# Performance work log

Measured on AMD Instinct MI355X. Metric: run time of the kernel, lower is better.

The kernel has to match this reference:

```python
import jax, jax.numpy as jnp
import numpy as np

HEADS = 16
KV_HEADS = 8
HEAD_DIM = 128
ROPE_BASE = 10000.0
RMS_EPS = 1e-5


def rmsnorm(x, w, eps=RMS_EPS):
    x = jnp.clip(x.astype(jnp.float32), -100.0, 100.0)
    var = jnp.clip(jnp.mean(x * x, axis=-1, keepdims=True), eps, None)
    x = x * jax.lax.rsqrt(var + eps)
    x = jnp.clip(x, -10.0, 10.0)
    return w * x


def activation_quant(x):
    x = jnp.clip(x, -50.0, 50.0)
    max_val = jnp.clip(jnp.max(jnp.abs(x), axis=-1, keepdims=True), 0.0001, None)
    scale = 127.0 / max_val
    return jnp.clip(jnp.round(x * scale), -128.0, 127.0) / scale


def weight_quant(w):
    scale = jnp.clip(jnp.mean(jnp.abs(w)), 1e-8, None)
    e = jnp.mean(w)
    return jnp.sign(w - e) * scale


def bitlinear(x, w, norm_w):
    xn = rmsnorm(x, norm_w)
    xq = xn + jax.lax.stop_gradient(activation_quant(xn) - xn)
    wq = w + jax.lax.stop_gradient(weight_quant(w) - w)
    return xq @ wq.T


def rope_tables(seq_len, dim):
    inv_freq = 1.0 / (ROPE_BASE ** (jnp.arange(0, dim, 2, dtype=jnp.float32) / dim))
    freqs = jnp.outer(jnp.arange(seq_len, dtype=jnp.float32), inv_freq)  # [S, dim/2]
    emb = jnp.concatenate([freqs, freqs], axis=-1)  # [S, dim]
    return jnp.cos(emb), jnp.sin(emb)


def rotate_half(x):
    x1, x2 = jnp.split(x, 2, axis=-1)
    return jnp.concatenate([-x2, x1], axis=-1)


def attention_forward(hidden_states, attention_mask, wq, wk, wv, wo, nq, nk, nv, no):
    B, S, H = hidden_states.shape
    q = bitlinear(hidden_states, wq, nq)  # [B,S,nh*hd]
    k = bitlinear(hidden_states, wk, nk)  # [B,S,nkv*hd]
    v = bitlinear(hidden_states, wv, nv)

    q = q.reshape(B, S, HEADS, HEAD_DIM).transpose(0, 2, 1, 3)       # [B,nh,S,hd]
    k = k.reshape(B, S, KV_HEADS, HEAD_DIM).transpose(0, 2, 1, 3)    # [B,nkv,S,hd]
    v = v.reshape(B, S, KV_HEADS, HEAD_DIM).transpose(0, 2, 1, 3)

    cos, sin = rope_tables(S, HEAD_DIM)
    cos = cos[None, None]  # [1,1,S,hd]
    sin = sin[None, None]
    q = q * cos + rotate_half(q) * sin
    k = k * cos + rotate_half(k) * sin

    groups = HEADS // KV_HEADS
    k_exp = jnp.repeat(k, groups, axis=1)  # [B,nh,S,hd]
    v_exp = jnp.repeat(v, groups, axis=1)

    scale = 1.0 / jnp.sqrt(jnp.float32(HEAD_DIM))
    scores = jnp.einsum('bhqd,bhkd->bhqk', q, k_exp) * scale
    scores = scores + attention_mask
    attn = jax.nn.softmax(scores, axis=-1)
    out = jnp.einsum('bhqk,bhkd->bhqd', attn, v_exp)
    out = out.transpose(0, 2, 1, 3).reshape(B, S, HEADS * HEAD_DIM)
    return bitlinear(out, wo, no)


def setup_inputs() -> dict:
    key = jax.random.key(0)
    ks = jax.random.split(key, 6)
    B, S, H = 2, 2048, 2048
    KVH = KV_HEADS * HEAD_DIM
    std = 0.02 / np.sqrt(H)
    return {
        'hidden_states': jax.random.normal(ks[0], (B, S, H), jnp.float32),
        'attention_mask': jnp.zeros((1, 1, S, S), jnp.float32),
        'wq': jax.random.normal(ks[1], (H, H), jnp.float32) * std,
        'wk': jax.random.normal(ks[2], (KVH, H), jnp.float32) * std,
        'wv': jax.random.normal(ks[3], (KVH, H), jnp.float32) * std,
        'wo': jax.random.normal(ks[4], (H, H), jnp.float32) * std,
        'nq': jnp.ones((H,), jnp.float32),
        'nk': jnp.ones((H,), jnp.float32),
        'nv': jnp.ones((H,), jnp.float32),
        'no': jnp.ones((H,), jnp.float32),
    }


def reference(hidden_states, attention_mask, wq, wk, wv, wo, nq, nk, nv, no):
    return attention_forward(hidden_states, attention_mask, wq, wk, wv, wo, nq, nk, nv, no)
```

## Files before the change

### kernel.cpp

```cpp
#include <hip/hip_runtime.h>


#define DI __device__ __forceinline__

using bf16   = __bf16;
using bf16x4 = __attribute__((ext_vector_type(4))) __bf16;
using bf16x8 = __attribute__((ext_vector_type(8))) __bf16;
using f32x4  = __attribute__((ext_vector_type(4))) float;

DI void gl_lds16(void* lds, const void* g) {
  __builtin_amdgcn_global_load_lds((const __attribute__((address_space(1))) void*)g,
                                   (__attribute__((address_space(3))) void*)lds, 16, 0, 0);
}
DI float clampf(float x, float lo, float hi) { return fminf(fmaxf(x, lo), hi); }

DI float block_sum(float v, float* red, int lane, int w) {
#pragma unroll
  for (int o = 32; o > 0; o >>= 1) v += __shfl_xor(v, o, 64);
  __syncthreads();
  if (lane == 0) red[w] = v;
  __syncthreads();
  return red[0] + red[1] + red[2] + red[3];
}
DI float block_max(float v, float* red, int lane, int w) {
#pragma unroll
  for (int o = 32; o > 0; o >>= 1) v = fmaxf(v, __shfl_xor(v, o, 64));
  __syncthreads();
  if (lane == 0) red[w] = v;
  __syncthreads();
  return fmaxf(fmaxf(red[0], red[1]), fmaxf(red[2], red[3]));
}

__global__ void wstats_kernel(const float* wq, const float* wk, const float* wv,
                              const float* wo, float* stats) {
  __shared__ float red[4], red2[4];
  int t = threadIdx.x, lane = t & 63, w = t >> 6;
  int m = blockIdx.y;
  const float* src; int n4;
  if (m == 0)      { src = wq; n4 = 1048576; }
  else if (m == 1) { src = wk; n4 = 524288;  }
  else if (m == 2) { src = wv; n4 = 524288;  }
  else             { src = wo; n4 = 1048576; }
  float s = 0.f, sa = 0.f;
  for (int i = blockIdx.x * 256 + t; i < n4; i += 256 * 256) {
    float4 v = ((const float4*)src)[i];
    s  += v.x + v.y + v.z + v.w;
    sa += fabsf(v.x) + fabsf(v.y) + fabsf(v.z) + fabsf(v.w);
  }
#pragma unroll
  for (int o = 32; o > 0; o >>= 1) { s += __shfl_xor(s, o, 64); sa += __shfl_xor(sa, o, 64); }
  if (lane == 0) { red[w] = s; red2[w] = sa; }
  __syncthreads();
  if (t == 0) {
    atomicAdd(&stats[2 * m],     red[0] + red[1] + red[2] + red[3]);
    atomicAdd(&stats[2 * m + 1], red2[0] + red2[1] + red2[2] + red2[3]);
  }
}

__global__ void wsign_kernel(const float* wq, const float* wk, const float* wv, const float* wo,
                             ushort* sq, ushort* sk, ushort* sv, ushort* so,
                             const float* stats) {
  int m = blockIdx.y;
  const float* src; ushort* dst; int n4; float cinv;
  if (m == 0)      { src = wq; dst = sq; n4 = 1048576; cinv = 1.f / 4194304.f; }
  else if (m == 1) { src = wk; dst = sk; n4 = 524288;  cinv = 1.f / 2097152.f; }
  else if (m == 2) { src = wv; dst = sv; n4 = 524288;  cinv = 1.f / 2097152.f; }
  else             { src = wo; dst = so; n4 = 1048576; cinv = 1.f / 4194304.f; }
  float e = stats[2 * m] * cinv;
  for (int i = blockIdx.x * 256 + threadIdx.x; i < n4; i += 1024 * 256) {
    float4 v = ((const float4*)src)[i];
    ushort4 o;
    o.x = v.x > e ? 0x3F80 : (v.x < e ? 0xBF80 : 0);
    o.y = v.y > e ? 0x3F80 : (v.y < e ? 0xBF80 : 0);
    o.z = v.z > e ? 0x3F80 : (v.z < e ? 0xBF80 : 0);
    o.w = v.w > e ? 0x3F80 : (v.w < e ? 0xBF80 : 0);
    ((ushort4*)dst)[i] = o;
  }
}

__global__ void ropetab_kernel(float* ct, float* st) {
  int s = blockIdx.x, j = threadIdx.x;
  float invf = powf(10000.f, -(float)j * (1.f / 64.f));
  float a = (float)s * invf;
  ct[s * 64 + j] = cosf(a);
  st[s * 64 + j] = sinf(a);
}

DI void quant_one(const float* xs, const float* __restrict__ wt, bf16* __restrict__ a,
                  float* __restrict__ r, int row, int t, int lane, int w, float* red) {
  float4 w0 = ((const float4*)wt)[t * 2], w1 = ((const float4*)wt)[t * 2 + 1];
  float wv[8] = {w0.x, w0.y, w0.z, w0.w, w1.x, w1.y, w1.z, w1.w};
  float y[8]; float am = 0.f;
#pragma unroll
  for (int e = 0; e < 8; ++e) {
    y[e] = clampf(wv[e] * xs[e], -50.f, 50.f);
    am = fmaxf(am, fabsf(y[e]));
  }
  float mx = block_max(am, red, lane, w);
  float maxval = fmaxf(mx, 1e-4f);
  float sc = 127.f / maxval;
  bf16x8 q;
#pragma unroll
  for (int e = 0; e < 8; ++e) {
    float n = rintf(y[e] * sc);
    n = clampf(n, -128.f, 127.f);
    q[e] = (bf16)n;
  }
  *(bf16x8*)(a + (size_t)row * 2048 + t * 8) = q;
  if (t == 0) r[row] = maxval * (1.f / 127.f);
}

template <int NW>
__launch_bounds__(256)
__global__ void rqnorm_kernel(const float* __restrict__ x,
                              const float* __restrict__ w0, const float* __restrict__ w1,
                              const float* __restrict__ w2,
                              bf16* a0, bf16* a1, bf16* a2,
                              float* r0, float* r1, float* r2) {
  __shared__ float red[4];
  int t = threadIdx.x, lane = t & 63, w = t >> 6;
  int row = blockIdx.x;
  const float* xr = x + (size_t)row * 2048;
  float4 u0 = ((const float4*)xr)[t * 2], u1 = ((const float4*)xr)[t * 2 + 1];
  float xs[8] = {u0.x, u0.y, u0.z, u0.w, u1.x, u1.y, u1.z, u1.w};
  float ss = 0.f;
#pragma unroll
  for (int e = 0; e < 8; ++e) { xs[e] = clampf(xs[e], -100.f, 100.f); ss += xs[e] * xs[e]; }
  float tot = block_sum(ss, red, lane, w);
  float var = fmaxf(tot * (1.f / 2048.f), 1e-5f);
  float inv = 1.f / sqrtf(var + 1e-5f);
#pragma unroll
  for (int e = 0; e < 8; ++e) xs[e] = clampf(xs[e] * inv, -10.f, 10.f);
  quant_one(xs, w0, a0, r0, row, t, lane, w, red);
  if (NW > 1) quant_one(xs, w1, a1, r1, row, t, lane, w, red);
  if (NW > 2) quant_one(xs, w2, a2, r2, row, t, lane, w, red);
}

DI void mm_core(const bf16* __restrict__ Ag0, const bf16* __restrict__ Bg0,
                bf16* As, bf16* Bs, int w, int lane, f32x4 acc[2][8]) {
  int l15 = lane & 15, quad = lane >> 4;
  int srow = w * 8 + (lane >> 3);
  int sc_p = (lane & 7) * 8;
  int sc_g = ((lane & 7) ^ (lane >> 3)) * 8;
  const bf16* Ag = Ag0 + (size_t)srow * 2048 + sc_g;
  const bf16* Bg = Bg0 + (size_t)srow * 2048 + sc_g;
  bf16* Al = As + srow * 64 + sc_p;
  bf16* Bl = Bs + srow * 64 + sc_p;
  for (int kt = 0; kt < 32; ++kt) {
    size_t kb = (size_t)kt * 64;
#pragma unroll
    for (int i = 0; i < 4; ++i) {
      gl_lds16(Al + i * 32 * 64, Ag + (size_t)i * 32 * 2048 + kb);
      gl_lds16(Bl + i * 32 * 64, Bg + (size_t)i * 32 * 2048 + kb);
    }
    __syncthreads();
#pragma unroll
    for (int kc = 0; kc < 2; ++kc) {
      bf16x8 af[2], bfr[8];
#pragma unroll
      for (int mt = 0; mt < 2; ++mt)
        af[mt] = *(const bf16x8*)(As + (w * 32 + mt * 16 + l15) * 64 +
                                  (((kc * 4 + quad) ^ (l15 & 7)) * 8));
#pragma unroll
      for (int nt = 0; nt < 8; ++nt)
        bfr[nt] = *(const bf16x8*)(Bs + (nt * 16 + l15) * 64 +
                                   (((kc * 4 + quad) ^ (l15 & 7)) * 8));
#pragma unroll
      for (int mt = 0; mt < 2; ++mt)
#pragma unroll
        for (int nt = 0; nt < 8; ++nt)
          acc[mt][nt] = __builtin_amdgcn_mfma_f32_16x16x32_bf16(af[mt], bfr[nt], acc[mt][nt], 0, 0, 0);
    }
    __syncthreads();
  }
}

__launch_bounds__(256, 2)
__global__ void qkv_gemm(const bf16* __restrict__ Aq, const bf16* __restrict__ Ak,
                         const bf16* __restrict__ Av, const bf16* __restrict__ Ball,
                         const float* __restrict__ rq, const float* __restrict__ rk,
                         const float* __restrict__ rv, const float* __restrict__ stats,
                         bf16* __restrict__ qr, bf16* __restrict__ kr,
                         float* __restrict__ vlin,
                         const float* __restrict__ ct, const float* __restrict__ st) {
  __shared__ bf16 As[128 * 64];
  __shared__ bf16 Bs[128 * 64];
  int t = threadIdx.x, w = t >> 6, lane = t & 63;
  int l15 = lane & 15, quad = lane >> 4;
  int x = blockIdx.x, m0 = blockIdx.y * 128;
  const bf16* A; const float* rs; float sw; int brow0;
  if (x < 16)      { A = Aq; rs = rq; sw = stats[1] * (1.f / 4194304.f); brow0 = x * 128; }
  else if (x < 24) { A = Ak; rs = rk; sw = stats[3] * (1.f / 2097152.f); brow0 = 2048 + (x - 16) * 128; }
  else             { A = Av; rs = rv; sw = stats[5] * (1.f / 2097152.f); brow0 = 3072 + (x - 24) * 128; }
  sw = fmaxf(sw, 1e-8f);
  f32x4 acc[2][8] = {};
  mm_core(A + (size_t)m0 * 2048, Ball + (size_t)brow0 * 2048, As, Bs, w, lane, acc);

  if (x < 24) {
    bf16* outb = (x < 16) ? qr : kr;
    int h = (x < 16) ? x : x - 16;
    int nh = (x < 16) ? 16 : 8;
#pragma unroll
    for (int mt = 0; mt < 2; ++mt)
#pragma unroll
      for (int r = 0; r < 4; ++r) {
        int row = m0 + w * 32 + mt * 16 + quad * 4 + r;
        float rsc = rs[row] * sw;
        int s = row & 2047, b = row >> 11;
        size_t base = ((size_t)(b * nh + h) * 2048 + s) * 128;
#pragma unroll
        for (int nt = 0; nt < 4; ++nt) {
          int d = nt * 16 + l15;
          float x1 = acc[mt][nt][r] * rsc;
          float x2 = acc[mt][nt + 4][r] * rsc;
          float c = ct[s * 64 + d], sn = st[s * 64 + d];
          outb[base + d]      = (bf16)(x1 * c - x2 * sn);
          outb[base + d + 64] = (bf16)(x2 * c + x1 * sn);
        }
      }
  } else {
    int n0 = (x - 24) * 128;
#pragma unroll
    for (int mt = 0; mt < 2; ++mt)
#pragma unroll
      for (int r = 0; r < 4; ++r) {
        int row = m0 + w * 32 + mt * 16 + quad * 4 + r;
        float rsc = rs[row] * sw;
#pragma unroll
        for (int nt = 0; nt < 8; ++nt)
          vlin[(size_t)row * 1024 + n0 + nt * 16 + l15] = acc[mt][nt][r] * rsc;
      }
  }
}

__launch_bounds__(256, 2)
__global__ void gemm_o(const bf16* __restrict__ A, const bf16* __restrict__ Bw,
                       const float* __restrict__ rs, const float* __restrict__ stats,
                       float* __restrict__ out) {
  __shared__ bf16 As[128 * 64];
  __shared__ bf16 Bs[128 * 64];
  int t = threadIdx.x, w = t >> 6, lane = t & 63;
  int l15 = lane & 15, quad = lane >> 4;
  int m0 = blockIdx.y * 128, n0 = blockIdx.x * 128;
  f32x4 acc[2][8] = {};
  mm_core(A + (size_t)m0 * 2048, Bw + (size_t)n0 * 2048, As, Bs, w, lane, acc);
  float sw = fmaxf(stats[7] * (1.f / 4194304.f), 1e-8f);
#pragma unroll
  for (int mt = 0; mt < 2; ++mt)
#pragma unroll
    for (int r = 0; r < 4; ++r) {
      int row = m0 + w * 32 + mt * 16 + quad * 4 + r;
      float rsc = rs[row] * sw;
#pragma unroll
      for (int nt = 0; nt < 8; ++nt)
        out[(size_t)row * 2048 + n0 + nt * 16 + l15] = acc[mt][nt][r] * rsc;
    }
}

__global__ void vtrans_kernel(const float* __restrict__ v_lin, bf16* __restrict__ v_t) {
  __shared__ float tile[64][65];
  int t = threadIdx.x, c = t & 63, rq = t >> 6;
  int ct0 = blockIdx.x * 64, tt0 = blockIdx.y * 64;
#pragma unroll
  for (int i = 0; i < 16; ++i) {
    int r = rq * 16 + i;
    tile[r][c] = v_lin[(size_t)(tt0 + r) * 1024 + ct0 + c];
  }
  __syncthreads();
  int token = tt0 + c;
  int b = token >> 11, s = token & 2047;
#pragma unroll
  for (int i = 0; i < 16; ++i) {
    int cg = ct0 + rq * 16 + i;
    int kvh = cg >> 7, d = cg & 127;
    v_t[((size_t)(b * 8 + kvh) * 128 + d) * 2048 + s] = (bf16)tile[c][rq * 16 + i];
  }
}

__launch_bounds__(256, 2)
__global__ void attn_kernel(const bf16* __restrict__ Q, const bf16* __restrict__ Kc,
                            const bf16* __restrict__ Vt, const float* __restrict__ mask,
                            float* __restrict__ Oout) {
  constexpr float scale = 0.08838834764831845f;
  __shared__ bf16 Ks[2][64 * 128];
  __shared__ bf16 Vs[2][128 * 64];
  __shared__ bf16 Ps[128 * 64];
  int t = threadIdx.x, w = t >> 6, lane = t & 63;
  int l15 = lane & 15, quad = lane >> 4;
  int bh = blockIdx.y, b = bh >> 4, h = bh & 15, kvh = h >> 1;
  int q0 = blockIdx.x * 128;
  const bf16* Qb = Q + (size_t)(b * 16 + h) * 2048 * 128;
  const bf16* Kb = Kc + (size_t)(b * 8 + kvh) * 2048 * 128;
  const bf16* Vb = Vt + (size_t)(b * 8 + kvh) * 128 * 2048;

  int qloc = w * 32 + l15;
  int qg = q0 + qloc;

  bf16x8 qf[2][4];
#pragma unroll
  for (int qt = 0; qt < 2; ++qt)
#pragma unroll
    for (int kc = 0; kc < 4; ++kc)
      qf[qt][kc] = *(const bf16x8*)(Qb + (size_t)(qg + qt * 16) * 128 + kc * 32 + quad * 8);

  f32x4 Oa[8][2] = {};
  float mrow[2] = {-1e30f, -1e30f}, lrow[2] = {0.f, 0.f};

  int krow = w * 4 + quad;
  int kcol_p = l15 * 8;
  int kcol_g = (l15 ^ krow) * 8;
  int vrow = w * 8 + (lane >> 3);
  int vc_p = (lane & 7) * 8;
  int vc_g = ((lane & 7) ^ (lane >> 3)) * 8;

  auto stage = [&](int buf, int kt) {
    int kk0 = kt * 64;
#pragma unroll
    for (int i = 0; i < 4; ++i)
      gl_lds16(&Ks[buf][(i * 16 + krow) * 128 + kcol_p],
               Kb + (size_t)(kk0 + i * 16 + krow) * 128 + kcol_g);
#pragma unroll
    for (int i = 0; i < 4; ++i)
      gl_lds16(&Vs[buf][(i * 32 + vrow) * 64 + vc_p],
               Vb + (size_t)(i * 32 + vrow) * 2048 + kk0 + vc_g);
  };

  stage(0, 0);

  f32x4 mv[2][4], mvn[2][4];
#pragma unroll
  for (int qt = 0; qt < 2; ++qt)
#pragma unroll
    for (int k2 = 0; k2 < 4; ++k2)
      mv[qt][k2] = *(const f32x4*)(mask + (size_t)(qg + qt * 16) * 2048 + k2 * 16 + quad * 4);

  for (int kt = 0; kt < 32; ++kt) {
    int cur = kt & 1;
    __syncthreads();
    if (kt < 31) stage(cur ^ 1, kt + 1);

    f32x4 Sacc[4][2] = {};
#pragma unroll
    for (int kc = 0; kc < 4; ++kc) {
      bf16x8 kf[4];
#pragma unroll
      for (int k2 = 0; k2 < 4; ++k2)
        kf[k2] = *(const bf16x8*)(&Ks[cur][(k2 * 16 + l15) * 128 + (((kc * 4 + quad) ^ l15) * 8)]);
#pragma unroll
      for (int k2 = 0; k2 < 4; ++k2)
#pragma unroll
        for (int qt = 0; qt < 2; ++qt)
          Sacc[k2][qt] = __builtin_amdgcn_mfma_f32_16x16x32_bf16(kf[k2], qf[qt][kc], Sacc[k2][qt], 0, 0, 0);
    }

#pragma unroll
    for (int qt = 0; qt < 2; ++qt) {
#pragma unroll
      for (int k2 = 0; k2 < 4; ++k2)
#pragma unroll
        for (int r = 0; r < 4; ++r)
          Sacc[k2][qt][r] = Sacc[k2][qt][r] * scale + mv[qt][k2][r];
      f32x4 vm = Sacc[0][qt];
#pragma unroll
      for (int k2 = 1; k2 < 4; ++k2)
#pragma unroll
        for (int r = 0; r < 4; ++r) vm[r] = fmaxf(vm[r], Sacc[k2][qt][r]);
      float mx = fmaxf(fmaxf(vm[0], vm[1]), fmaxf(vm[2], vm[3]));
      mx = fmaxf(mx, __shfl_xor(mx, 16, 64));
      mx = fmaxf(mx, __shfl_xor(mx, 32, 64));
      float mnew = fmaxf(mrow[qt], mx);
      float alpha = __expf(mrow[qt] - mnew);
      mrow[qt] = mnew;
      f32x4 vs = {0.f, 0.f, 0.f, 0.f};
#pragma unroll
      for (int k2 = 0; k2 < 4; ++k2)
#pragma unroll
        for (int r = 0; r < 4; ++r) {
          float p = __expf(Sacc[k2][qt][r] - mnew);
          Sacc[k2][qt][r] = p;
          vs[r] += p;
        }
      float rsum = (vs[0] + vs[1]) + (vs[2] + vs[3]);
      rsum += __shfl_xor(rsum, 16, 64);
      rsum += __shfl_xor(rsum, 32, 64);
      lrow[qt] = lrow[qt] * alpha + rsum;
#pragma unroll
      for (int dt = 0; dt < 8; ++dt) Oa[dt][qt] *= alpha;
      int qr = qloc + qt * 16;
#pragma unroll
      for (int k2 = 0; k2 < 4; ++k2) {
        bf16x4 pk;
#pragma unroll
        for (int r = 0; r < 4; ++r) pk[r] = (bf16)Sacc[k2][qt][r];
        int c = k2 * 2 + (quad >> 1);
        *(bf16x4*)(&Ps[qr * 64 + ((c ^ (qr & 7)) * 8) + (quad & 1) * 4]) = pk;
      }
    }

    if (kt < 31) {
      int kk1 = (kt + 1) * 64;
#pragma unroll
      for (int qt = 0; qt < 2; ++qt)
#pragma unroll
        for (int k2 = 0; k2 < 4; ++k2)
          mvn[qt][k2] = *(const f32x4*)(mask + (size_t)(qg + qt * 16) * 2048 + kk1 + k2 * 16 + quad * 4);
    }

#pragma unroll
    for (int kc = 0; kc < 2; ++kc) {
      bf16x8 pf[2];
#pragma unroll
      for (int qt = 0; qt < 2; ++qt)
        pf[qt] = *(const bf16x8*)(&Ps[(qloc + qt * 16) * 64 + (((kc * 4 + quad) ^ (l15 & 7)) * 8)]);
#pragma unroll
      for (int dt = 0; dt < 8; ++dt) {
        bf16x8 vf = *(const bf16x8*)(&Vs[cur][(dt * 16 + l15) * 64 +
                                              (((kc * 4 + quad) ^ (l15 & 7)) * 8)]);
#pragma unroll
        for (int qt = 0; qt < 2; ++qt)
          Oa[dt][qt] = __builtin_amdgcn_mfma_f32_16x16x32_bf16(vf, pf[qt], Oa[dt][qt], 0, 0, 0);
      }
    }

#pragma unroll
    for (int qt = 0; qt < 2; ++qt)
#pragma unroll
      for (int k2 = 0; k2 < 4; ++k2) mv[qt][k2] = mvn[qt][k2];
  }

#pragma unroll
  for (int qt = 0; qt < 2; ++qt) {
    float inv = 1.f / lrow[qt];
    int token = b * 2048 + qg + qt * 16;
#pragma unroll
    for (int dt = 0; dt < 8; ++dt) {
      f32x4 o = Oa[dt][qt] * inv;
      *(f32x4*)(Oout + (size_t)token * 2048 + h * 128 + dt * 16 + quad * 4) = o;
    }
  }
}

extern "C" void kernel_launch(void* const* d_in, const int* in_sizes, int n_in,
                              void* d_out, int out_size, void* d_ws, size_t ws_size,
                              hipStream_t stream) {
  const float* hidden = (const float*)d_in[0];
  const float* mask   = (const float*)d_in[1];
  const float* wq = (const float*)d_in[2];
  const float* wk = (const float*)d_in[3];
  const float* wv = (const float*)d_in[4];
  const float* wo = (const float*)d_in[5];
  const float* nq = (const float*)d_in[6];
  const float* nk = (const float*)d_in[7];
  const float* nv = (const float*)d_in[8];
  const float* no = (const float*)d_in[9];
  float* out = (float*)d_out;
  char* ws = (char*)d_ws;

  constexpr size_t O_STATS = 0;
  constexpr size_t O_CT    = 256;
  constexpr size_t O_ST    = O_CT + 524288;
  constexpr size_t O_SQ    = O_ST + 524288;
  constexpr size_t O_SK    = O_SQ + 8388608;
  constexpr size_t O_SV    = O_SK + 4194304;
  constexpr size_t O_SO    = O_SV + 4194304;
  constexpr size_t O_RSQ   = O_SO + 8388608;
  constexpr size_t O_RSK   = O_RSQ + 16384;
  constexpr size_t O_RSV   = O_RSK + 16384;
  constexpr size_t O_RSO   = O_RSV + 16384;
  constexpr size_t O_AQQ   = O_RSO + 16384;
  constexpr size_t O_AQK   = O_AQQ + 16777216;
  constexpr size_t O_AQV   = O_AQK + 16777216;
  constexpr size_t O_QR    = O_AQV + 16777216;
  constexpr size_t O_KR    = O_QR + 16777216;
  constexpr size_t O_VT    = O_KR + 8388608;
  constexpr size_t O_VLIN2 = O_VT + 8388608;
  constexpr size_t O_ATTN  = O_AQQ;
  constexpr size_t O_AQO   = O_AQV;

  float* stats = (float*)(ws + O_STATS);
  float* ct = (float*)(ws + O_CT);
  float* st = (float*)(ws + O_ST);

  (void)hipMemsetAsync(ws + O_STATS, 0, 256, stream);

  wstats_kernel<<<dim3(256, 4), 256, 0, stream>>>(wq, wk, wv, wo, stats);
  wsign_kernel<<<dim3(1024, 4), 256, 0, stream>>>(wq, wk, wv, wo,
      (ushort*)(ws + O_SQ), (ushort*)(ws + O_SK), (ushort*)(ws + O_SV), (ushort*)(ws + O_SO), stats);
  ropetab_kernel<<<dim3(2048), 64, 0, stream>>>(ct, st);

  rqnorm_kernel<3><<<dim3(4096), 256, 0, stream>>>(hidden, nq, nk, nv,
      (bf16*)(ws + O_AQQ), (bf16*)(ws + O_AQK), (bf16*)(ws + O_AQV),
      (float*)(ws + O_RSQ), (float*)(ws + O_RSK), (float*)(ws + O_RSV));

  qkv_gemm<<<dim3(32, 32), 256, 0, stream>>>(
      (const bf16*)(ws + O_AQQ), (const bf16*)(ws + O_AQK), (const bf16*)(ws + O_AQV),
      (const bf16*)(ws + O_SQ),
      (const float*)(ws + O_RSQ), (const float*)(ws + O_RSK), (const float*)(ws + O_RSV),
      stats, (bf16*)(ws + O_QR), (bf16*)(ws + O_KR), (float*)(ws + O_VLIN2), ct, st);

  vtrans_kernel<<<dim3(16, 64), 256, 0, stream>>>((const float*)(ws + O_VLIN2), (bf16*)(ws + O_VT));

  attn_kernel<<<dim3(16, 32), 256, 0, stream>>>(
      (const bf16*)(ws + O_QR), (const bf16*)(ws + O_KR), (const bf16*)(ws + O_VT),
      mask, (float*)(ws + O_ATTN));

  rqnorm_kernel<1><<<dim3(4096), 256, 0, stream>>>((const float*)(ws + O_ATTN), no, no, no,
      (bf16*)(ws + O_AQO), (bf16*)(ws + O_AQO), (bf16*)(ws + O_AQO),
      (float*)(ws + O_RSO), (float*)(ws + O_RSO), (float*)(ws + O_RSO));

  gemm_o<<<dim3(16, 32), 256, 0, stream>>>(
      (const bf16*)(ws + O_AQO), (const bf16*)(ws + O_SO), (float*)(ws + O_RSO), stats, out);

  (void)in_sizes; (void)n_in; (void)out_size; (void)ws_size;
}
```

Measured before the change: 437.3 us.

## Fuse V transpose into QKV GEMM epilogue and shrink attention tiles

The V projection epilogue now writes bf16 directly in the transposed [b,kvh,d,s] layout, which removes the fp32 intermediate buffer and the separate transpose kernel. The attention kernel moves from 128 to 64 query rows per block and from 64 to 32 keys per iteration. That gives one query tile per wave, less LDS per block, launch bounds raised to 4 blocks per SM, and twice as many blocks. The cost is more loop iterations, more K/V reloads per query (each block covers fewer queries), and smaller MFMA batches per sync.

```diff
diff --git a/kernel.cpp b/kernel.cpp
--- a/kernel.cpp
+++ b/kernel.cpp
@@ -181,7 +181,7 @@
                          const float* __restrict__ rq, const float* __restrict__ rk,
                          const float* __restrict__ rv, const float* __restrict__ stats,
                          bf16* __restrict__ qr, bf16* __restrict__ kr,
-                         float* __restrict__ vlin,
+                         bf16* __restrict__ vt_out,
                          const float* __restrict__ ct, const float* __restrict__ st) {
   __shared__ bf16 As[128 * 64];
   __shared__ bf16 Bs[128 * 64];
@@ -219,17 +219,24 @@
         }
       }
   } else {
-    int n0 = (x - 24) * 128;
-#pragma unroll
-    for (int mt = 0; mt < 2; ++mt)
-#pragma unroll
-      for (int r = 0; r < 4; ++r) {
-        int row = m0 + w * 32 + mt * 16 + quad * 4 + r;
-        float rsc = rs[row] * sw;
-#pragma unroll
-        for (int nt = 0; nt < 8; ++nt)
-          vlin[(size_t)row * 1024 + n0 + nt * 16 + l15] = acc[mt][nt][r] * rsc;
+    int n0x = (x - 24) * 128;
+#pragma unroll
+    for (int mt = 0; mt < 2; ++mt) {
+      int token0 = m0 + w * 32 + mt * 16 + quad * 4;
+      float rsc[4];
+#pragma unroll
+      for (int r = 0; r < 4; ++r) rsc[r] = rs[token0 + r] * sw;
+      int bb = token0 >> 11, s0 = token0 & 2047;
+#pragma unroll
+      for (int nt = 0; nt < 8; ++nt) {
+        int col = n0x + nt * 16 + l15;
+        int kvh2 = col >> 7, d = col & 127;
+        bf16x4 pv;
+#pragma unroll
+        for (int r = 0; r < 4; ++r) pv[r] = (bf16)(acc[mt][nt][r] * rsc[r]);
+        *(bf16x4*)(vt_out + ((size_t)(bb * 8 + kvh2) * 128 + d) * 2048 + s0) = pv;
       }
+    }
   }
 }
 
@@ -257,186 +264,137 @@
     }
 }
 
-__global__ void vtrans_kernel(const float* __restrict__ v_lin, bf16* __restrict__ v_t) {
-  __shared__ float tile[64][65];
-  int t = threadIdx.x, c = t & 63, rq = t >> 6;
-  int ct0 = blockIdx.x * 64, tt0 = blockIdx.y * 64;
-#pragma unroll
-  for (int i = 0; i < 16; ++i) {
-    int r = rq * 16 + i;
-    tile[r][c] = v_lin[(size_t)(tt0 + r) * 1024 + ct0 + c];
-  }
-  __syncthreads();
-  int token = tt0 + c;
-  int b = token >> 11, s = token & 2047;
-#pragma unroll
-  for (int i = 0; i < 16; ++i) {
-    int cg = ct0 + rq * 16 + i;
-    int kvh = cg >> 7, d = cg & 127;
-    v_t[((size_t)(b * 8 + kvh) * 128 + d) * 2048 + s] = (bf16)tile[c][rq * 16 + i];
-  }
-}
-
-__launch_bounds__(256, 2)
+__launch_bounds__(256, 4)
 __global__ void attn_kernel(const bf16* __restrict__ Q, const bf16* __restrict__ Kc,
                             const bf16* __restrict__ Vt, const float* __restrict__ mask,
                             float* __restrict__ Oout) {
   constexpr float scale = 0.08838834764831845f;
-  __shared__ bf16 Ks[2][64 * 128];
-  __shared__ bf16 Vs[2][128 * 64];
-  __shared__ bf16 Ps[128 * 64];
+  __shared__ bf16 Ks[2][32 * 128];
+  __shared__ bf16 Vs[2][128 * 32];
+  __shared__ bf16 Ps[64 * 40];
   int t = threadIdx.x, w = t >> 6, lane = t & 63;
   int l15 = lane & 15, quad = lane >> 4;
   int bh = blockIdx.y, b = bh >> 4, h = bh & 15, kvh = h >> 1;
-  int q0 = blockIdx.x * 128;
+  int q0 = blockIdx.x * 64;
   const bf16* Qb = Q + (size_t)(b * 16 + h) * 2048 * 128;
   const bf16* Kb = Kc + (size_t)(b * 8 + kvh) * 2048 * 128;
   const bf16* Vb = Vt + (size_t)(b * 8 + kvh) * 128 * 2048;
 
-  int qloc = w * 32 + l15;
+  int qloc = w * 16 + l15;
   int qg = q0 + qloc;
 
-  bf16x8 qf[2][4];
-#pragma unroll
-  for (int qt = 0; qt < 2; ++qt)
-#pragma unroll
-    for (int kc = 0; kc < 4; ++kc)
-      qf[qt][kc] = *(const bf16x8*)(Qb + (size_t)(qg + qt * 16) * 128 + kc * 32 + quad * 8);
-
-  f32x4 Oa[8][2] = {};
-  float mrow[2] = {-1e30f, -1e30f}, lrow[2] = {0.f, 0.f};
-
-  int krow = w * 4 + quad;
-  int kcol_p = l15 * 8;
-  int kcol_g = (l15 ^ krow) * 8;
-  int vrow = w * 8 + (lane >> 3);
-  int vc_p = (lane & 7) * 8;
-  int vc_g = ((lane & 7) ^ (lane >> 3)) * 8;
+  bf16x8 qf[4];
+#pragma unroll
+  for (int kc = 0; kc < 4; ++kc)
+    qf[kc] = *(const bf16x8*)(Qb + (size_t)qg * 128 + kc * 32 + quad * 8);
+
+  f32x4 Oa[8] = {};
+  float mrow = -1e30f, lrow = 0.f;
+
+  int ksr = t >> 4;
+  int ksc_p = (t & 15) * 8;
+  int ksc_g = ((t & 15) ^ ksr) * 8;
+  int vsr = t >> 2;
+  int vsc_p = (t & 3) * 8;
+  int vsc_g = ((t & 3) ^ (vsr & 3)) * 8;
 
   auto stage = [&](int buf, int kt) {
-    int kk0 = kt * 64;
-#pragma unroll
-    for (int i = 0; i < 4; ++i)
-      gl_lds16(&Ks[buf][(i * 16 + krow) * 128 + kcol_p],
-               Kb + (size_t)(kk0 + i * 16 + krow) * 128 + kcol_g);
-#pragma unroll
-    for (int i = 0; i < 4; ++i)
-      gl_lds16(&Vs[buf][(i * 32 + vrow) * 64 + vc_p],
-               Vb + (size_t)(i * 32 + vrow) * 2048 + kk0 + vc_g);
+    int kk0 = kt * 32;
+#pragma unroll
+    for (int i = 0; i < 2; ++i)
+      gl_lds16(&Ks[buf][(i * 16 + ksr) * 128 + ksc_p],
+               Kb + (size_t)(kk0 + i * 16 + ksr) * 128 + ksc_g);
+#pragma unroll
+    for (int i = 0; i < 2; ++i)
+      gl_lds16(&Vs[buf][(i * 64 + vsr) * 32 + vsc_p],
+               Vb + (size_t)(i * 64 + vsr) * 2048 + kk0 + vsc_g);
   };
 
   stage(0, 0);
 
-  f32x4 mv[2][4], mvn[2][4];
-#pragma unroll
-  for (int qt = 0; qt < 2; ++qt)
-#pragma unroll
-    for (int k2 = 0; k2 < 4; ++k2)
-      mv[qt][k2] = *(const f32x4*)(mask + (size_t)(qg + qt * 16) * 2048 + k2 * 16 + quad * 4);
-
-  for (int kt = 0; kt < 32; ++kt) {
+  f32x4 mv[2], mvn[2];
+#pragma unroll
+  for (int k2 = 0; k2 < 2; ++k2)
+    mv[k2] = *(const f32x4*)(mask + (size_t)qg * 2048 + k2 * 16 + quad * 4);
+
+  for (int kt = 0; kt < 64; ++kt) {
     int cur = kt & 1;
     __syncthreads();
-    if (kt < 31) stage(cur ^ 1, kt + 1);
-
-    f32x4 Sacc[4][2] = {};
+    if (kt < 63) stage(cur ^ 1, kt + 1);
+
+    f32x4 Sacc[2] = {};
 #pragma unroll
     for (int kc = 0; kc < 4; ++kc) {
-      bf16x8 kf[4];
-#pragma unroll
-      for (int k2 = 0; k2 < 4; ++k2)
+      bf16x8 kf[2];
+#pragma unroll
+      for (int k2 = 0; k2 < 2; ++k2)
         kf[k2] = *(const bf16x8*)(&Ks[cur][(k2 * 16 + l15) * 128 + (((kc * 4 + quad) ^ l15) * 8)]);
 #pragma unroll
-      for (int k2 = 0; k2 < 4; ++k2)
-#pragma unroll
-        for (int qt = 0; qt < 2; ++qt)
-          Sacc[k2][qt] = __builtin_amdgcn_mfma_f32_16x16x32_bf16(kf[k2], qf[qt][kc], Sacc[k2][qt], 0, 0, 0);
-    }
-
-#pragma unroll
-    for (int qt = 0; qt < 2; ++qt) {
-#pragma unroll
-      for (int k2 = 0; k2 < 4; ++k2)
-#pragma unroll
-        for (int r = 0; r < 4; ++r)
-          Sacc[k2][qt][r] = Sacc[k2][qt][r] * scale + mv[qt][k2][r];
-      f32x4 vm = Sacc[0][qt];
-#pragma unroll
-      for (int k2 = 1; k2 < 4; ++k2)
-#pragma unroll
-        for (int r = 0; r < 4; ++r) vm[r] = fmaxf(vm[r], Sacc[k2][qt][r]);
-      float mx = fmaxf(fmaxf(vm[0], vm[1]), fmaxf(vm[2], vm[3]));
-      mx = fmaxf(mx, __shfl_xor(mx, 16, 64));
-      mx = fmaxf(mx, __shfl_xor(mx, 32, 64));
-      float mnew = fmaxf(mrow[qt], mx);
-      float alpha = __expf(mrow[qt] - mnew);
-      mrow[qt] = mnew;
-      f32x4 vs = {0.f, 0.f, 0.f, 0.f};
-#pragma unroll
-      for (int k2 = 0; k2 < 4; ++k2)
-#pragma unroll
-        for (int r = 0; r < 4; ++r) {
-          float p = __expf(Sacc[k2][qt][r] - mnew);
-          Sacc[k2][qt][r] = p;
-          vs[r] += p;
-        }
-      float rsum = (vs[0] + vs[1]) + (vs[2] + vs[3]);
-      rsum += __shfl_xor(rsum, 16, 64);
-      rsum += __shfl_xor(rsum, 32, 64);
-      lrow[qt] = lrow[qt] * alpha + rsum;
-#pragma unroll
-      for (int dt = 0; dt < 8; ++dt) Oa[dt][qt] *= alpha;
-      int qr = qloc + qt * 16;
-#pragma unroll
-      for (int k2 = 0; k2 < 4; ++k2) {
-        bf16x4 pk;
-#pragma unroll
-        for (int r = 0; r < 4; ++r) pk[r] = (bf16)Sacc[k2][qt][r];
-        int c = k2 * 2 + (quad >> 1);
-        *(bf16x4*)(&Ps[qr * 64 + ((c ^ (qr & 7)) * 8) + (quad & 1) * 4]) = pk;
+      for (int k2 = 0; k2 < 2; ++k2)
+        Sacc[k2] = __builtin_amdgcn_mfma_f32_16x16x32_bf16(kf[k2], qf[kc], Sacc[k2], 0, 0, 0);
+    }
+
+    if (kt < 63) {
+      int kk1 = (kt + 1) * 32;
+#pragma unroll
+      for (int k2 = 0; k2 < 2; ++k2)
+        mvn[k2] = *(const f32x4*)(mask + (size_t)qg * 2048 + kk1 + k2 * 16 + quad * 4);
+    }
+
+#pragma unroll
+    for (int k2 = 0; k2 < 2; ++k2)
+#pragma unroll
+      for (int r = 0; r < 4; ++r)
+        Sacc[k2][r] = Sacc[k2][r] * scale + mv[k2][r];
+    f32x4 vm;
+#pragma unroll
+    for (int r = 0; r < 4; ++r) vm[r] = fmaxf(Sacc[0][r], Sacc[1][r]);
+    float mx = fmaxf(fmaxf(vm[0], vm[1]), fmaxf(vm[2], vm[3]));
+    mx = fmaxf(mx, __shfl_xor(mx, 16, 64));
+    mx = fmaxf(mx, __shfl_xor(mx, 32, 64));
+    float mnew = fmaxf(mrow, mx);
+    float alpha = __expf(mrow - mnew);
+    mrow = mnew;
+    f32x4 vs = {0.f, 0.f, 0.f, 0.f};
+#pragma unroll
+    for (int k2 = 0; k2 < 2; ++k2)
+#pragma unroll
+      for (int r = 0; r < 4; ++r) {
+        float p = __expf(Sacc[k2][r] - mnew);
+        Sacc[k2][r] = p;
+        vs[r] += p;
       }
-    }
-
-    if (kt < 31) {
-      int kk1 = (kt + 1) * 64;
-#pragma unroll
-      for (int qt = 0; qt < 2; ++qt)
-#pragma unroll
-        for (int k2 = 0; k2 < 4; ++k2)
-          mvn[qt][k2] = *(const f32x4*)(mask + (size_t)(qg + qt * 16) * 2048 + kk1 + k2 * 16 + quad * 4);
-    }
-
-#pragma unroll
-    for (int kc = 0; kc < 2; ++kc) {
-      bf16x8 pf[2];
-#pragma unroll
-      for (int qt = 0; qt < 2; ++qt)
-        pf[qt] = *(const bf16x8*)(&Ps[(qloc + qt * 16) * 64 + (((kc * 4 + quad) ^ (l15 & 7)) * 8)]);
-#pragma unroll
-      for (int dt = 0; dt < 8; ++dt) {
-        bf16x8 vf = *(const bf16x8*)(&Vs[cur][(dt * 16 + l15) * 64 +
-                                              (((kc * 4 + quad) ^ (l15 & 7)) * 8)]);
-#pragma unroll
-        for (int qt = 0; qt < 2; ++qt)
-          Oa[dt][qt] = __builtin_amdgcn_mfma_f32_16x16x32_bf16(vf, pf[qt], Oa[dt][qt], 0, 0, 0);
-      }
-    }
-
-#pragma unroll
-    for (int qt = 0; qt < 2; ++qt)
-#pragma unroll
-      for (int k2 = 0; k2 < 4; ++k2) mv[qt][k2] = mvn[qt][k2];
-  }
-
-#pragma unroll
-  for (int qt = 0; qt < 2; ++qt) {
-    float inv = 1.f / lrow[qt];
-    int token = b * 2048 + qg + qt * 16;
+    float rsum = (vs[0] + vs[1]) + (vs[2] + vs[3]);
+    rsum += __shfl_xor(rsum, 16, 64);
+    rsum += __shfl_xor(rsum, 32, 64);
+    lrow = lrow * alpha + rsum;
+#pragma unroll
+    for (int dt = 0; dt < 8; ++dt) Oa[dt] *= alpha;
+#pragma unroll
+    for (int k2 = 0; k2 < 2; ++k2) {
+      bf16x4 pk;
+#pragma unroll
+      for (int r = 0; r < 4; ++r) pk[r] = (bf16)Sacc[k2][r];
+      *(bf16x4*)(&Ps[qloc * 40 + k2 * 16 + quad * 4]) = pk;
+    }
+
+    bf16x8 pf = *(const bf16x8*)(&Ps[qloc * 40 + quad * 8]);
 #pragma unroll
     for (int dt = 0; dt < 8; ++dt) {
-      f32x4 o = Oa[dt][qt] * inv;
-      *(f32x4*)(Oout + (size_t)token * 2048 + h * 128 + dt * 16 + quad * 4) = o;
-    }
+      bf16x8 vf = *(const bf16x8*)(&Vs[cur][(dt * 16 + l15) * 32 + ((quad ^ (l15 & 3)) * 8)]);
+      Oa[dt] = __builtin_amdgcn_mfma_f32_16x16x32_bf16(vf, pf, Oa[dt], 0, 0, 0);
+    }
+
+#pragma unroll
+    for (int k2 = 0; k2 < 2; ++k2) mv[k2] = mvn[k2];
+  }
+
+  float inv = 1.f / lrow;
+  int token = b * 2048 + qg;
+#pragma unroll
+  for (int dt = 0; dt < 8; ++dt) {
+    f32x4 o = Oa[dt] * inv;
+    *(f32x4*)(Oout + (size_t)token * 2048 + h * 128 + dt * 16 + quad * 4) = o;
   }
 }
 
@@ -473,7 +431,6 @@
   constexpr size_t O_QR    = O_AQV + 16777216;
   constexpr size_t O_KR    = O_QR + 16777216;
   constexpr size_t O_VT    = O_KR + 8388608;
-  constexpr size_t O_VLIN2 = O_VT + 8388608;
   constexpr size_t O_ATTN  = O_AQQ;
   constexpr size_t O_AQO   = O_AQV;
 
@@ -496,11 +453,9 @@
       (const bf16*)(ws + O_AQQ), (const bf16*)(ws + O_AQK), (const bf16*)(ws + O_AQV),
       (const bf16*)(ws + O_SQ),
       (const float*)(ws + O_RSQ), (const float*)(ws + O_RSK), (const float*)(ws + O_RSV),
-      stats, (bf16*)(ws + O_QR), (bf16*)(ws + O_KR), (float*)(ws + O_VLIN2), ct, st);
-
-  vtrans_kernel<<<dim3(16, 64), 256, 0, stream>>>((const float*)(ws + O_VLIN2), (bf16*)(ws + O_VT));
-
-  attn_kernel<<<dim3(16, 32), 256, 0, stream>>>(
+      stats, (bf16*)(ws + O_QR), (bf16*)(ws + O_KR), (bf16*)(ws + O_VT), ct, st);
+
+  attn_kernel<<<dim3(32, 32), 256, 0, stream>>>(
       (const bf16*)(ws + O_QR), (const bf16*)(ws + O_KR), (const bf16*)(ws + O_VT),
       mask, (float*)(ws + O_ATTN));
 
```

New measurement: 444.8 us. About the same (+1.7%).
